# Performance work log

Measured on AMD Instinct MI355X. Metric: run time of the kernel, lower is better.

## Reference

```python
import jax, jax.numpy as jnp
import numpy as np

T, N, D, E = 4, 50000, 32, 800000
V_TH = 1.0      # v_threshold
ALPHA = 4.0     # surrogate-gradient sharpness


def setup_inputs() -> dict:
    key = jax.random.key(0)
    k1, k2, k3, k4 = jax.random.split(key, 4)
    s_seq = jax.random.normal(k1, (T, N, D), dtype=jnp.float32) * 0.5
    z_seq = jax.random.normal(k2, (N, D), dtype=jnp.float32) * 0.5
    edge_index = jax.random.randint(k3, (2, E), 0, N, dtype=jnp.int64)
    # GCNConv weight (bias=False), Glorot-ish scale
    W = jax.random.normal(k4, (D, D), dtype=jnp.float32) / np.sqrt(D).astype(np.float32)
    return {"s_seq": s_seq, "z_seq": z_seq, "W": W, "edge_index": edge_index}


def _gcn_conv(x, W, edge_index, n_nodes):
    """PyG GCNConv with add_self_loops=True, normalize=True, bias=False.
    x: [T,N,D]; returns [T,N,D]."""
    src, dst = edge_index[0], edge_index[1]
    ones = jnp.ones(src.shape[0], dtype=x.dtype)
    deg = jax.ops.segment_sum(ones, dst, num_segments=n_nodes) + 1.0  # +1 self loop
    dinv = jax.lax.rsqrt(deg)                                        # [N]
    xw = jnp.einsum('tnd,df->tnf', x, W)                             # dense transform
    norm = dinv[src] * dinv[dst]                                     # [E]
    msgs = xw[:, src, :] * norm[None, :, None]                       # [T,E,D] gather
    agg = jax.vmap(lambda m: jax.ops.segment_sum(m, dst, num_segments=n_nodes))(msgs)
    # self-loop contribution with norm dinv[i]^2
    return agg + xw * (dinv * dinv)[None, :, None]


def _spike(v):
    # Heaviside spike with surrogate (sigmoid) gradient, straight-through.
    s = (v >= V_TH).astype(v.dtype)
    sg = jax.nn.sigmoid(ALPHA * (v - V_TH))
    return s + sg - jax.lax.stop_gradient(sg)


def reference(s_seq, z_seq, W, edge_index):
    n_nodes = s_seq.shape[1]
    x_seq = _gcn_conv(s_seq, W, edge_index, n_nodes)   # [T,N,D]  (dropout p=0.0 is identity)
    y_seq = x_seq.mean(0)                              # temporal mean [N,D]
    # Riemannian IF node: integrate-and-fire over time with soft reset;
    # latent state z drifts by the temporal mean (Euclidean proxy for expmap).
    def step(v, x_t):
        v = v + x_t
        o = _spike(v)
        v = v - o * V_TH
        return v, o
    v0 = jnp.zeros_like(z_seq)
    _, o_seq = jax.lax.scan(step, v0, x_seq)           # [T,N,D]
    z_new = z_seq + y_seq
    return o_seq, z_new
```

## Files before the change

kernel.cpp:

```cpp
#include <hip/hip_runtime.h>
#include <hip/hip_fp16.h>

#define TSTEPS 4
#define DIM 32
#define BINW_SHIFT 8
#define NB 256
#define SP_CH 2048
#define PAD_PER_BIN 772

typedef _Float16 f16x8 __attribute__((ext_vector_type(8)));
typedef float f32x4 __attribute__((ext_vector_type(4)));

__device__ __forceinline__ void ldx8h(const __half* p, float4& lo, float4& hi) {
    uint4 u = *(const uint4*)p;
    __half2 h0 = *(__half2*)&u.x;
    __half2 h1 = *(__half2*)&u.y;
    __half2 h2 = *(__half2*)&u.z;
    __half2 h3 = *(__half2*)&u.w;
    float2 a = __half22float2(h0);
    float2 b = __half22float2(h1);
    float2 c = __half22float2(h2);
    float2 d = __half22float2(h3);
    lo = make_float4(a.x, a.y, b.x, b.y);
    hi = make_float4(c.x, c.y, d.x, d.y);
}

__global__ __launch_bounds__(256) void histgemm_kernel(
    const int* __restrict__ ei, int* __restrict__ ghist,
    const float* __restrict__ s, const float* __restrict__ W,
    __half* __restrict__ xwp, int E, int rows, int N, int nchunks) {
    __shared__ float Wf[32][33];
    int tid = threadIdx.x;

    if ((int)blockIdx.x < nchunks) {
        int* lh = (int*)Wf;
        lh[tid] = 0;
        __syncthreads();
        int beg = blockIdx.x * SP_CH;
        int end = min(beg + SP_CH, E);
        for (int e = beg + tid; e < end; e += 256)
            atomicAdd(&lh[ei[E + e] >> BINW_SHIFT], 1);
        __syncthreads();
        ghist[(size_t)blockIdx.x * NB + tid] = lh[tid];
        return;
    }

    {
        float4 wv = ((const float4*)W)[tid];
        int kk = tid >> 3, c4 = (tid & 7) * 4;
        Wf[kk][c4 + 0] = wv.x; Wf[kk][c4 + 1] = wv.y;
        Wf[kk][c4 + 2] = wv.z; Wf[kk][c4 + 3] = wv.w;
    }
    __syncthreads();

    int lane = tid & 63;
    int wid  = tid >> 6;
    int lrow = lane & 15;
    int kq   = lane >> 4;
    int k0   = kq * 8;

    f16x8 b0, b1;
#pragma unroll
    for (int i = 0; i < 8; i++) {
        b0[i] = (_Float16)Wf[k0 + i][lrow];
        b1[i] = (_Float16)Wf[k0 + i][lrow + 16];
    }

    int rbase = ((int)blockIdx.x - nchunks) * 128 + wid * 32;
#pragma unroll
    for (int rt = 0; rt < 2; rt++) {
        int r = rbase + rt * 16 + lrow;
        f16x8 a;
        if (r < rows) {
            const float4* sp = (const float4*)(s + (size_t)r * 32 + k0);
            float4 u0 = sp[0], u1 = sp[1];
            a[0] = (_Float16)u0.x; a[1] = (_Float16)u0.y;
            a[2] = (_Float16)u0.z; a[3] = (_Float16)u0.w;
            a[4] = (_Float16)u1.x; a[5] = (_Float16)u1.y;
            a[6] = (_Float16)u1.z; a[7] = (_Float16)u1.w;
        } else {
#pragma unroll
            for (int i = 0; i < 8; i++) a[i] = (_Float16)0.f;
        }
        f32x4 c0 = {0.f, 0.f, 0.f, 0.f};
        f32x4 c1 = {0.f, 0.f, 0.f, 0.f};
        c0 = __builtin_amdgcn_mfma_f32_16x16x32_f16(b0, a, c0, 0, 0, 0);
        c1 = __builtin_amdgcn_mfma_f32_16x16x32_f16(b1, a, c1, 0, 0, 0);
        if (r < rows) {
            int t = (r >= 3 * N) ? 3 : (r >= 2 * N) ? 2 : (r >= N) ? 1 : 0;
            int n = r - t * N;
            __half2 p0 = __floats2half2_rn(c0[0], c0[1]);
            __half2 p1 = __floats2half2_rn(c0[2], c0[3]);
            __half2 p2 = __floats2half2_rn(c1[0], c1[1]);
            __half2 p3 = __floats2half2_rn(c1[2], c1[3]);
            __half* dst = xwp + (size_t)n * 128 + t * 32;
            uint2 u0, u1;
            u0.x = *(unsigned int*)&p0; u0.y = *(unsigned int*)&p1;
            u1.x = *(unsigned int*)&p2; u1.y = *(unsigned int*)&p3;
            *(uint2*)(dst + kq * 4)      = u0;
            *(uint2*)(dst + 16 + kq * 4) = u1;
        }
    }
}

__global__ __launch_bounds__(512) void colscan_kernel(
    const int* __restrict__ ghist, int* __restrict__ ghist2,
    int* __restrict__ totals, int nchunks) {
    __shared__ int sc[512];
    int t = threadIdx.x;
    int b = blockIdx.x;
    int v = (t < nchunks) ? ghist[(size_t)t * NB + b] : 0;
    sc[t] = v;
    __syncthreads();
    for (int off = 1; off < 512; off <<= 1) {
        int tv = (t >= off) ? sc[t - off] : 0;
        __syncthreads();
        sc[t] += tv;
        __syncthreads();
    }
    if (t < nchunks) ghist2[(size_t)t * NB + b] = sc[t] - v;
    if (t == 511) totals[b] = sc[511];
}

__global__ __launch_bounds__(256) void split_kernel(
    const int* __restrict__ ei, const int* __restrict__ ghist,
    const int* __restrict__ ghist2, const int* __restrict__ totals,
    unsigned int* __restrict__ esorted, int E) {
    __shared__ int binB[NB], pscan[NB], gb[NB], pcur[NB];
    __shared__ unsigned int sbuf[SP_CH];
    int tid = threadIdx.x;
    int bid = blockIdx.x;

    int tot = totals[tid];
    binB[tid] = tot;
    __syncthreads();
    for (int off = 1; off < 256; off <<= 1) {
        int t = (tid >= off) ? binB[tid - off] : 0;
        __syncthreads();
        binB[tid] += t;
        __syncthreads();
    }
    int v = ghist[(size_t)bid * NB + tid];
    pscan[tid] = v;
    __syncthreads();
    for (int off = 1; off < 256; off <<= 1) {
        int t = (tid >= off) ? pscan[tid - off] : 0;
        __syncthreads();
        pscan[tid] += t;
        __syncthreads();
    }
    int pexcl = pscan[tid] - v;
    pscan[tid] = pexcl;
    pcur[tid] = pexcl;
    gb[tid] = (binB[tid] - tot) + ghist2[(size_t)bid * NB + tid] - pexcl;
    __syncthreads();

    int beg = bid * SP_CH;
    int end = min(beg + SP_CH, E);
    int cnt = end - beg;
    for (int e = beg + tid; e < end; e += 256) {
        int sx = ei[e];
        int dx = ei[E + e];
        unsigned int pk = (unsigned int)sx | ((unsigned int)dx << 16);
        int b = dx >> BINW_SHIFT;
        int p = atomicAdd(&pcur[b], 1);
        sbuf[p] = pk;
    }
    __syncthreads();
    for (int idx = tid; idx < cnt; idx += 256) {
        unsigned int e = sbuf[idx];
        int b = e >> 24;
        esorted[gb[b] + idx] = e;
    }
}

__global__ __launch_bounds__(256) void csr_kernel(
    const int* __restrict__ totals, const unsigned int* __restrict__ esorted,
    int* __restrict__ rec, int* __restrict__ offs, int* __restrict__ deg,
    float* __restrict__ dinv, __half* __restrict__ xwp, int N) {
    __shared__ int lh[NB], sc[NB], loff[NB], lcur[NB];
    __shared__ float sdi[NB];
    __shared__ int s_ebeg, s_cnt;
    int bin = blockIdx.x;
    int tid = threadIdx.x;
    sc[tid] = totals[tid];
    lh[tid] = 0;
    __syncthreads();
    for (int off = 1; off < 256; off <<= 1) {
        int t = (tid >= off) ? sc[tid - off] : 0;
        __syncthreads();
        sc[tid] += t;
        __syncthreads();
    }
    if (tid == 0) {
        int e0 = bin ? sc[bin - 1] : 0;
        s_ebeg = e0;
        s_cnt = sc[bin] - e0;
    }
    __syncthreads();
    int ebeg = s_ebeg;
    int cnt = s_cnt;
    int gbase = ((ebeg + 3) & ~3) + PAD_PER_BIN * bin;
    for (int i = tid; i < cnt; i += 256)
        atomicAdd(&lh[(esorted[ebeg + i] >> 16) & 255], 1);
    __syncthreads();
    sdi[tid] = rsqrtf((float)lh[tid] + 1.0f);
    int padded = (lh[tid] + 3) & ~3;
    sc[tid] = padded;
    __syncthreads();
    for (int off = 1; off < 256; off <<= 1) {
        int t = (tid >= off) ? sc[tid - off] : 0;
        __syncthreads();
        sc[tid] += t;
        __syncthreads();
    }
    loff[tid] = sc[tid] - padded;
    lcur[tid] = 0;
    __syncthreads();
    for (int i = tid; i < cnt; i += 256) {
        unsigned int e = esorted[ebeg + i];
        int ln = (e >> 16) & 255;
        int p = atomicAdd(&lcur[ln], 1);
        rec[gbase + loff[ln] + p] = (int)(e & 0xFFFFu);
    }
    int n = (bin << BINW_SHIFT) + tid;
    if (n < N) {
        offs[n] = gbase + loff[tid];
        deg[n] = lh[tid];
        dinv[n] = sdi[tid];
    }
    {
        int hbase = bin << 15;
        int limit = min(32768, N * 128 - hbase);
        __half* slab = xwp + hbase;
        for (int i = tid; i * 8 < limit; i += 256) {
            float di = sdi[i >> 4];
            uint4 u = *(uint4*)(slab + i * 8);
            __half2 h0 = *(__half2*)&u.x;
            __half2 h1 = *(__half2*)&u.y;
            __half2 h2 = *(__half2*)&u.z;
            __half2 h3 = *(__half2*)&u.w;
            float2 f0 = __half22float2(h0);
            float2 f1 = __half22float2(h1);
            float2 f2 = __half22float2(h2);
            float2 f3 = __half22float2(h3);
            h0 = __floats2half2_rn(f0.x * di, f0.y * di);
            h1 = __floats2half2_rn(f1.x * di, f1.y * di);
            h2 = __floats2half2_rn(f2.x * di, f2.y * di);
            h3 = __floats2half2_rn(f3.x * di, f3.y * di);
            u.x = *(unsigned int*)&h0;
            u.y = *(unsigned int*)&h1;
            u.z = *(unsigned int*)&h2;
            u.w = *(unsigned int*)&h3;
            *(uint4*)(slab + i * 8) = u;
        }
    }
}

__global__ __launch_bounds__(256) void gather_kernel(
    const int* __restrict__ rec, const int* __restrict__ offs,
    const int* __restrict__ deg, const __half* __restrict__ xwp,
    const float* __restrict__ dinv, const float* __restrict__ z,
    float* __restrict__ out, int N) {
    int gid = blockIdx.x * 256 + threadIdx.x;
    int n = gid >> 4;
    if (n >= N) return;
    int wl = threadIdx.x & 63;
    int g = wl >> 4;
    int l = wl & 15;
    long lofs = (long)l * 8;

    float dn = dinv[n];
    int beg = offs[n];
    int cntn = deg[n];

    float4 aLo = make_float4(0.f, 0.f, 0.f, 0.f);
    float4 aHi = make_float4(0.f, 0.f, 0.f, 0.f);
    int i = 0;
    for (; i + 8 <= cntn; i += 8) {
        int4 sa = *(const int4*)(rec + beg + i);
        int4 sb = *(const int4*)(rec + beg + i + 4);
        float4 l0, h0, l1, h1, l2, h2, l3, h3;
        float4 l4, h4, l5, h5, l6, h6, l7, h7;
        ldx8h(xwp + (long)sa.x * 128 + lofs, l0, h0);
        ldx8h(xwp + (long)sa.y * 128 + lofs, l1, h1);
        ldx8h(xwp + (long)sa.z * 128 + lofs, l2, h2);
        ldx8h(xwp + (long)sa.w * 128 + lofs, l3, h3);
        ldx8h(xwp + (long)sb.x * 128 + lofs, l4, h4);
        ldx8h(xwp + (long)sb.y * 128 + lofs, l5, h5);
        ldx8h(xwp + (long)sb.z * 128 + lofs, l6, h6);
        ldx8h(xwp + (long)sb.w * 128 + lofs, l7, h7);
        aLo.x += (l0.x + l1.x) + (l2.x + l3.x) + (l4.x + l5.x) + (l6.x + l7.x);
        aLo.y += (l0.y + l1.y) + (l2.y + l3.y) + (l4.y + l5.y) + (l6.y + l7.y);
        aLo.z += (l0.z + l1.z) + (l2.z + l3.z) + (l4.z + l5.z) + (l6.z + l7.z);
        aLo.w += (l0.w + l1.w) + (l2.w + l3.w) + (l4.w + l5.w) + (l6.w + l7.w);
        aHi.x += (h0.x + h1.x) + (h2.x + h3.x) + (h4.x + h5.x) + (h6.x + h7.x);
        aHi.y += (h0.y + h1.y) + (h2.y + h3.y) + (h4.y + h5.y) + (h6.y + h7.y);
        aHi.z += (h0.z + h1.z) + (h2.z + h3.z) + (h4.z + h5.z) + (h6.z + h7.z);
        aHi.w += (h0.w + h1.w) + (h2.w + h3.w) + (h4.w + h5.w) + (h6.w + h7.w);
    }
    for (; i < cntn; i += 4) {
        int4 s4 = *(const int4*)(rec + beg + i);
        int rem = cntn - i;
        int i0 = s4.x;
        int i1 = (rem > 1) ? s4.y : i0;
        int i2 = (rem > 2) ? s4.z : i0;
        int i3 = (rem > 3) ? s4.w : i0;
        float w1 = (rem > 1) ? 1.f : 0.f;
        float w2 = (rem > 2) ? 1.f : 0.f;
        float w3 = (rem > 3) ? 1.f : 0.f;
        float4 l0, h0, l1, h1, l2, h2, l3, h3;
        ldx8h(xwp + (long)i0 * 128 + lofs, l0, h0);
        ldx8h(xwp + (long)i1 * 128 + lofs, l1, h1);
        ldx8h(xwp + (long)i2 * 128 + lofs, l2, h2);
        ldx8h(xwp + (long)i3 * 128 + lofs, l3, h3);
        aLo.x += l0.x + w1 * l1.x + w2 * l2.x + w3 * l3.x;
        aLo.y += l0.y + w1 * l1.y + w2 * l2.y + w3 * l3.y;
        aLo.z += l0.z + w1 * l1.z + w2 * l2.z + w3 * l3.z;
        aLo.w += l0.w + w1 * l1.w + w2 * l2.w + w3 * l3.w;
        aHi.x += h0.x + w1 * h1.x + w2 * h2.x + w3 * h3.x;
        aHi.y += h0.y + w1 * h1.y + w2 * h2.y + w3 * h3.y;
        aHi.z += h0.z + w1 * h1.z + w2 * h2.z + w3 * h3.z;
        aHi.w += h0.w + w1 * h1.w + w2 * h2.w + w3 * h3.w;
    }
    {
        float4 sl, sh;
        ldx8h(xwp + (long)n * 128 + lofs, sl, sh);
        aLo.x += sl.x; aLo.y += sl.y; aLo.z += sl.z; aLo.w += sl.w;
        aHi.x += sh.x; aHi.y += sh.y; aHi.z += sh.z; aHi.w += sh.w;
    }
    aLo.x *= dn; aLo.y *= dn; aLo.z *= dn; aLo.w *= dn;
    aHi.x *= dn; aHi.y *= dn; aHi.z *= dn; aHi.w *= dn;

    float a8[8] = {aLo.x, aLo.y, aLo.z, aLo.w, aHi.x, aHi.y, aHi.z, aHi.w};
    float xs[TSTEPS][8];
    int base = g * 16;
#pragma unroll
    for (int t = 0; t < TSTEPS; t++) {
        int srcLane = base + t * 4 + l;
#pragma unroll
        for (int j = 0; j < 8; j++)
            xs[t][j] = __shfl(a8[j], srcLane, 64);
    }
    if (l < 4) {
        int colBase = n * 32 + l * 8;
        float v[8], y[8];
#pragma unroll
        for (int j = 0; j < 8; j++) {
            v[j] = 0.f;
            y[j] = (xs[0][j] + xs[1][j] + xs[2][j] + xs[3][j]) * 0.25f;
        }
#pragma unroll
        for (int t = 0; t < TSTEPS; t++) {
            float o[8];
#pragma unroll
            for (int j = 0; j < 8; j++) {
                v[j] += xs[t][j];
                o[j] = (v[j] >= 1.0f) ? 1.0f : 0.0f;
                v[j] -= o[j];
            }
            float* dst = out + (size_t)t * N * 32 + colBase;
            *(float4*)dst       = make_float4(o[0], o[1], o[2], o[3]);
            *(float4*)(dst + 4) = make_float4(o[4], o[5], o[6], o[7]);
        }
        float4 zv0 = *(const float4*)(z + colBase);
        float4 zv1 = *(const float4*)(z + colBase + 4);
        float* dst = out + (size_t)TSTEPS * N * 32 + colBase;
        *(float4*)dst       = make_float4(zv0.x + y[0], zv0.y + y[1], zv0.z + y[2], zv0.w + y[3]);
        *(float4*)(dst + 4) = make_float4(zv1.x + y[4], zv1.y + y[5], zv1.z + y[6], zv1.w + y[7]);
    }
}

extern "C" void kernel_launch(void* const* d_in, const int* in_sizes, int n_in,
                              void* d_out, int out_size, void* d_ws, size_t ws_size,
                              hipStream_t stream) {
    const float* s_seq = (const float*)d_in[0];
    const float* z_seq = (const float*)d_in[1];
    const float* W     = (const float*)d_in[2];
    const int*   ei    = (const int*)d_in[3];
    float* out = (float*)d_out;

    int N = in_sizes[1] / DIM;
    int E = in_sizes[3] / 2;
    int rows = TSTEPS * N;
    int nb = (N + 255) >> BINW_SHIFT;
    int nchunks = (E + SP_CH - 1) / SP_CH;

    char* w = (char*)d_ws;
    __half* xwp           = (__half*)w;       w += (size_t)rows * DIM * 2;
    unsigned int* esorted = (unsigned int*)w; w += (size_t)E * 4;
    int*   rec    = (int*)w;  w += ((size_t)E + PAD_PER_BIN * nb + 16) * 4;
    int*   offs   = (int*)w;  w += (size_t)N * 4;
    int*   deg    = (int*)w;  w += (size_t)N * 4;
    float* dinv   = (float*)w; w += (size_t)N * 4;
    int*   ghist  = (int*)w;  w += (size_t)nchunks * NB * 4;
    int*   ghist2 = (int*)w;  w += (size_t)nchunks * NB * 4;
    int*   totals = (int*)w;  w += NB * 4;

    int xwBlocks = (rows + 127) / 128;
    histgemm_kernel<<<nchunks + xwBlocks, 256, 0, stream>>>(
        ei, ghist, s_seq, W, xwp, E, rows, N, nchunks);
    colscan_kernel<<<NB, 512, 0, stream>>>(ghist, ghist2, totals, nchunks);
    split_kernel<<<nchunks, 256, 0, stream>>>(ei, ghist, ghist2, totals, esorted, E);
    csr_kernel<<<nb, 256, 0, stream>>>(totals, esorted, rec, offs, deg, dinv, xwp, N);
    gather_kernel<<<(N * 16 + 255) / 256, 256, 0, stream>>>(rec, offs, deg, xwp,
                                                            dinv, z_seq, out, N);
}
```

Measured before the change: 154.2 us.

## Fuse edge split with GEMM, transpose histogram, simplify split scatter

Moves the dense XW GEMM out of the histogram kernel and into the split kernel, so the GEMM blocks run alongside the edge scatter instead of alongside the histogram. The histogram is stored transposed so the column scan reads contiguous memory. The split phase drops the local per-chunk prefix scan and shared staging buffer and scatters straight to global positions, which gives up ordered coalesced writes in exchange for fewer passes and barriers. The bin prefix is computed once and passed to the CSR kernel, which now uses 512 threads. The NCHP=400 stride caps the number of chunks.

```diff
diff --git a/kernel.cpp b/kernel.cpp
--- a/kernel.cpp
+++ b/kernel.cpp
@@ -6,6 +6,7 @@
 #define BINW_SHIFT 8
 #define NB 256
 #define SP_CH 2048
+#define NCHP 400
 #define PAD_PER_BIN 772
 
 typedef _Float16 f16x8 __attribute__((ext_vector_type(8)));
@@ -25,26 +26,80 @@
     hi = make_float4(c.x, c.y, d.x, d.y);
 }
 
-__global__ __launch_bounds__(256) void histgemm_kernel(
-    const int* __restrict__ ei, int* __restrict__ ghist,
+__global__ __launch_bounds__(256) void hist_kernel(
+    const int* __restrict__ ei, int* __restrict__ ghistT, int E) {
+    __shared__ int lh[NB];
+    int tid = threadIdx.x;
+    lh[tid] = 0;
+    __syncthreads();
+    int beg = blockIdx.x * SP_CH;
+    int end = min(beg + SP_CH, E);
+    for (int e = beg + tid; e < end; e += 256)
+        atomicAdd(&lh[ei[E + e] >> BINW_SHIFT], 1);
+    __syncthreads();
+    ghistT[tid * NCHP + blockIdx.x] = lh[tid];
+}
+
+__global__ __launch_bounds__(512) void colscan_kernel(
+    const int* __restrict__ ghistT, int* __restrict__ ghist2,
+    int* __restrict__ totals, int nchunks) {
+    __shared__ int sc[512];
+    int t = threadIdx.x;
+    int b = blockIdx.x;
+    int v = (t < nchunks) ? ghistT[b * NCHP + t] : 0;
+    sc[t] = v;
+    __syncthreads();
+    for (int off = 1; off < 512; off <<= 1) {
+        int tv = (t >= off) ? sc[t - off] : 0;
+        __syncthreads();
+        sc[t] += tv;
+        __syncthreads();
+    }
+    if (t < nchunks) ghist2[(size_t)t * NB + b] = sc[t] - v;
+    if (t == 511) totals[b] = sc[511];
+}
+
+__global__ __launch_bounds__(256) void splitgemm_kernel(
+    const int* __restrict__ ei, const int* __restrict__ ghist2,
+    const int* __restrict__ totals, unsigned int* __restrict__ esorted,
+    int* __restrict__ binScanG,
     const float* __restrict__ s, const float* __restrict__ W,
     __half* __restrict__ xwp, int E, int rows, int N, int nchunks) {
-    __shared__ float Wf[32][33];
+    __shared__ __align__(16) char smem[4352];
     int tid = threadIdx.x;
 
     if ((int)blockIdx.x < nchunks) {
-        int* lh = (int*)Wf;
-        lh[tid] = 0;
-        __syncthreads();
-        int beg = blockIdx.x * SP_CH;
+        int* sBS  = (int*)smem;
+        int* gb   = (int*)(smem + 1024);
+        int* lcur = (int*)(smem + 2048);
+        int bid = blockIdx.x;
+        int tot = totals[tid];
+        sBS[tid] = tot;
+        __syncthreads();
+        for (int off = 1; off < 256; off <<= 1) {
+            int t = (tid >= off) ? sBS[tid - off] : 0;
+            __syncthreads();
+            sBS[tid] += t;
+            __syncthreads();
+        }
+        if (bid == 0) binScanG[tid] = sBS[tid];
+        gb[tid] = (sBS[tid] - tot) + ghist2[(size_t)bid * NB + tid];
+        lcur[tid] = 0;
+        __syncthreads();
+        int beg = bid * SP_CH;
         int end = min(beg + SP_CH, E);
-        for (int e = beg + tid; e < end; e += 256)
-            atomicAdd(&lh[ei[E + e] >> BINW_SHIFT], 1);
-        __syncthreads();
-        ghist[(size_t)blockIdx.x * NB + tid] = lh[tid];
+        for (int e = beg + tid; e < end; e += 256) {
+            int sx = ei[e];
+            int dx = ei[E + e];
+            unsigned int pk = (unsigned int)sx | ((unsigned int)dx << 16);
+            int b = dx >> BINW_SHIFT;
+            int p = atomicAdd(&lcur[b], 1);
+            esorted[gb[b] + p] = pk;
+        }
         return;
     }
 
+    float (*Wf)[33] = (float(*)[33])smem;
     {
         float4 wv = ((const float4*)W)[tid];
         int kk = tid >> 3, c4 = (tid & 7) * 4;
@@ -103,128 +158,50 @@
     }
 }
 
-__global__ __launch_bounds__(512) void colscan_kernel(
-    const int* __restrict__ ghist, int* __restrict__ ghist2,
-    int* __restrict__ totals, int nchunks) {
-    __shared__ int sc[512];
-    int t = threadIdx.x;
-    int b = blockIdx.x;
-    int v = (t < nchunks) ? ghist[(size_t)t * NB + b] : 0;
-    sc[t] = v;
-    __syncthreads();
-    for (int off = 1; off < 512; off <<= 1) {
-        int tv = (t >= off) ? sc[t - off] : 0;
-        __syncthreads();
-        sc[t] += tv;
-        __syncthreads();
-    }
-    if (t < nchunks) ghist2[(size_t)t * NB + b] = sc[t] - v;
-    if (t == 511) totals[b] = sc[511];
-}
-
-__global__ __launch_bounds__(256) void split_kernel(
-    const int* __restrict__ ei, const int* __restrict__ ghist,
-    const int* __restrict__ ghist2, const int* __restrict__ totals,
-    unsigned int* __restrict__ esorted, int E) {
-    __shared__ int binB[NB], pscan[NB], gb[NB], pcur[NB];
-    __shared__ unsigned int sbuf[SP_CH];
-    int tid = threadIdx.x;
-    int bid = blockIdx.x;
-
-    int tot = totals[tid];
-    binB[tid] = tot;
-    __syncthreads();
-    for (int off = 1; off < 256; off <<= 1) {
-        int t = (tid >= off) ? binB[tid - off] : 0;
-        __syncthreads();
-        binB[tid] += t;
-        __syncthreads();
-    }
-    int v = ghist[(size_t)bid * NB + tid];
-    pscan[tid] = v;
-    __syncthreads();
-    for (int off = 1; off < 256; off <<= 1) {
-        int t = (tid >= off) ? pscan[tid - off] : 0;
-        __syncthreads();
-        pscan[tid] += t;
-        __syncthreads();
-    }
-    int pexcl = pscan[tid] - v;
-    pscan[tid] = pexcl;
-    pcur[tid] = pexcl;
-    gb[tid] = (binB[tid] - tot) + ghist2[(size_t)bid * NB + tid] - pexcl;
-    __syncthreads();
-
-    int beg = bid * SP_CH;
-    int end = min(beg + SP_CH, E);
-    int cnt = end - beg;
-    for (int e = beg + tid; e < end; e += 256) {
-        int sx = ei[e];
-        int dx = ei[E + e];
-        unsigned int pk = (unsigned int)sx | ((unsigned int)dx << 16);
-        int b = dx >> BINW_SHIFT;
-        int p = atomicAdd(&pcur[b], 1);
-        sbuf[p] = pk;
-    }
-    __syncthreads();
-    for (int idx = tid; idx < cnt; idx += 256) {
-        unsigned int e = sbuf[idx];
-        int b = e >> 24;
-        esorted[gb[b] + idx] = e;
-    }
-}
-
-__global__ __launch_bounds__(256) void csr_kernel(
-    const int* __restrict__ totals, const unsigned int* __restrict__ esorted,
+__global__ __launch_bounds__(512) void csr_kernel(
+    const int* __restrict__ binScanG, const unsigned int* __restrict__ esorted,
     int* __restrict__ rec, int* __restrict__ offs, int* __restrict__ deg,
     float* __restrict__ dinv, __half* __restrict__ xwp, int N) {
     __shared__ int lh[NB], sc[NB], loff[NB], lcur[NB];
     __shared__ float sdi[NB];
-    __shared__ int s_ebeg, s_cnt;
     int bin = blockIdx.x;
     int tid = threadIdx.x;
-    sc[tid] = totals[tid];
-    lh[tid] = 0;
+    int e0 = bin ? binScanG[bin - 1] : 0;
+    int e1 = binScanG[bin];
+    int ebeg = e0;
+    int cnt = e1 - e0;
+    if (tid < NB) lh[tid] = 0;
+    __syncthreads();
+    int gbase = ((ebeg + 3) & ~3) + PAD_PER_BIN * bin;
+    for (int i = tid; i < cnt; i += 512)
+        atomicAdd(&lh[(esorted[ebeg + i] >> 16) & 255], 1);
+    __syncthreads();
+    int padded = 0;
+    if (tid < NB) {
+        sdi[tid] = rsqrtf((float)lh[tid] + 1.0f);
+        padded = (lh[tid] + 3) & ~3;
+        sc[tid] = padded;
+    }
     __syncthreads();
     for (int off = 1; off < 256; off <<= 1) {
-        int t = (tid >= off) ? sc[tid - off] : 0;
-        __syncthreads();
-        sc[tid] += t;
-        __syncthreads();
-    }
-    if (tid == 0) {
-        int e0 = bin ? sc[bin - 1] : 0;
-        s_ebeg = e0;
-        s_cnt = sc[bin] - e0;
-    }
-    __syncthreads();
-    int ebeg = s_ebeg;
-    int cnt = s_cnt;
-    int gbase = ((ebeg + 3) & ~3) + PAD_PER_BIN * bin;
-    for (int i = tid; i < cnt; i += 256)
-        atomicAdd(&lh[(esorted[ebeg + i] >> 16) & 255], 1);
-    __syncthreads();
-    sdi[tid] = rsqrtf((float)lh[tid] + 1.0f);
-    int padded = (lh[tid] + 3) & ~3;
-    sc[tid] = padded;
-    __syncthreads();
-    for (int off = 1; off < 256; off <<= 1) {
-        int t = (tid >= off) ? sc[tid - off] : 0;
-        __syncthreads();
-        sc[tid] += t;
-        __syncthreads();
-    }
-    loff[tid] = sc[tid] - padded;
-    lcur[tid] = 0;
-    __syncthreads();
-    for (int i = tid; i < cnt; i += 256) {
+        int t = (tid >= off && tid < NB) ? sc[tid - off] : 0;
+        __syncthreads();
+        if (tid < NB) sc[tid] += t;
+        __syncthreads();
+    }
+    if (tid < NB) {
+        loff[tid] = sc[tid] - padded;
+        lcur[tid] = 0;
+    }
+    __syncthreads();
+    for (int i = tid; i < cnt; i += 512) {
         unsigned int e = esorted[ebeg + i];
         int ln = (e >> 16) & 255;
         int p = atomicAdd(&lcur[ln], 1);
         rec[gbase + loff[ln] + p] = (int)(e & 0xFFFFu);
     }
     int n = (bin << BINW_SHIFT) + tid;
-    if (n < N) {
+    if (tid < NB && n < N) {
         offs[n] = gbase + loff[tid];
         deg[n] = lh[tid];
         dinv[n] = sdi[tid];
@@ -233,7 +210,7 @@
         int hbase = bin << 15;
         int limit = min(32768, N * 128 - hbase);
         __half* slab = xwp + hbase;
-        for (int i = tid; i * 8 < limit; i += 256) {
+        for (int i = tid; i * 8 < limit; i += 512) {
             float di = sdi[i >> 4];
             uint4 u = *(uint4*)(slab + i * 8);
             __half2 h0 = *(__half2*)&u.x;
@@ -389,20 +366,22 @@
     char* w = (char*)d_ws;
     __half* xwp           = (__half*)w;       w += (size_t)rows * DIM * 2;
     unsigned int* esorted = (unsigned int*)w; w += (size_t)E * 4;
-    int*   rec    = (int*)w;  w += ((size_t)E + PAD_PER_BIN * nb + 16) * 4;
-    int*   offs   = (int*)w;  w += (size_t)N * 4;
-    int*   deg    = (int*)w;  w += (size_t)N * 4;
-    float* dinv   = (float*)w; w += (size_t)N * 4;
-    int*   ghist  = (int*)w;  w += (size_t)nchunks * NB * 4;
-    int*   ghist2 = (int*)w;  w += (size_t)nchunks * NB * 4;
-    int*   totals = (int*)w;  w += NB * 4;
+    int*   rec     = (int*)w;  w += ((size_t)E + PAD_PER_BIN * nb + 16) * 4;
+    int*   offs    = (int*)w;  w += (size_t)N * 4;
+    int*   deg     = (int*)w;  w += (size_t)N * 4;
+    float* dinv    = (float*)w; w += (size_t)N * 4;
+    int*   ghistT  = (int*)w;  w += (size_t)NB * NCHP * 4;
+    int*   ghist2  = (int*)w;  w += (size_t)nchunks * NB * 4;
+    int*   totals  = (int*)w;  w += NB * 4;
+    int*   binScanG = (int*)w; w += NB * 4;
 
     int xwBlocks = (rows + 127) / 128;
-    histgemm_kernel<<<nchunks + xwBlocks, 256, 0, stream>>>(
-        ei, ghist, s_seq, W, xwp, E, rows, N, nchunks);
-    colscan_kernel<<<NB, 512, 0, stream>>>(ghist, ghist2, totals, nchunks);
-    split_kernel<<<nchunks, 256, 0, stream>>>(ei, ghist, ghist2, totals, esorted, E);
-    csr_kernel<<<nb, 256, 0, stream>>>(totals, esorted, rec, offs, deg, dinv, xwp, N);
+    hist_kernel<<<nchunks, 256, 0, stream>>>(ei, ghistT, E);
+    colscan_kernel<<<NB, 512, 0, stream>>>(ghistT, ghist2, totals, nchunks);
+    splitgemm_kernel<<<nchunks + xwBlocks, 256, 0, stream>>>(
+        ei, ghist2, totals, esorted, binScanG, s_seq, W, xwp, E, rows, N, nchunks);
+    csr_kernel<<<nb, 512, 0, stream>>>(binScanG, esorted, rec, offs, deg, dinv,
+                                       xwp, N);
     gather_kernel<<<(N * 16 + 255) / 256, 256, 0, stream>>>(rec, offs, deg, xwp,
                                                             dinv, z_seq, out, N);
 }
```

New measurement: 151.1 us. -2.0%, faster.
